# Kernel tuning notes

Measured on AMD Instinct MI355X. Metric: run time of the kernel, lower is better.

## Reference

```python
import jax, jax.numpy as jnp
import numpy as np

NUM_EMBEDDINGS = 1024
EMBEDDING_DIM = 64
COMMITMENT_WEIGHT = 0.25
BATCH = 262144


def setup_inputs() -> dict:
    key = jax.random.key(0)
    k1, k2 = jax.random.split(key)
    z = jax.random.normal(k1, (BATCH, EMBEDDING_DIM), dtype=jnp.float32)
    # torch init: uniform_(-1/K, 1/K)
    bound = 1.0 / NUM_EMBEDDINGS
    codebook = jax.random.uniform(k2, (NUM_EMBEDDINGS, EMBEDDING_DIM), dtype=jnp.float32,
                                  minval=-bound, maxval=bound)
    return {"z": z, "codebook": codebook}


def reference(z, codebook):
    # distances[b, k] = ||z_b||^2 - 2 z_b . c_k + ||c_k||^2   -> [B, K]
    z2 = jnp.sum(z * z, axis=1, keepdims=True)                 # [B, 1]
    c2 = jnp.sum(codebook * codebook, axis=1)                  # [K]
    cross = jnp.matmul(z, codebook.T)                          # [B, K]
    distances = z2 - 2.0 * cross + c2
    indices = jnp.argmin(distances, axis=1)                    # [B]
    # original uses one-hot @ codebook; direct gather is the same math
    z_q = codebook[indices]                                    # [B, D]
    commitment_loss = jnp.mean((jax.lax.stop_gradient(z_q) - z) ** 2)
    codebook_loss = jnp.mean((z_q - jax.lax.stop_gradient(z)) ** 2)
    vq_loss = codebook_loss + COMMITMENT_WEIGHT * commitment_loss
    # straight-through estimator
    z_q_st = z + jax.lax.stop_gradient(z_q - z)
    return z_q_st, vq_loss, indices
```

## Files before the change

kernel.cpp:

```cpp
#include <hip/hip_runtime.h>

#define BATCH   262144
#define NCODE   1024
#define DIM     64
#define BLOCK   256
#define NBLK    (BATCH / BLOCK)
#define MARGIN  4e-5f
#define QCAP    65536


typedef __attribute__((ext_vector_type(8))) short bf16x8;
typedef __attribute__((ext_vector_type(4))) float f32x4;

#define MFMA(a, b, c) __builtin_amdgcn_mfma_f32_16x16x32_bf16(a, b, c, 0, 0, 0)

__device__ __forceinline__ void split1(float f, unsigned short& h, unsigned short& l) {
    unsigned u = __float_as_uint(f);
    unsigned r = (u + 0x7fffu + ((u >> 16) & 1u)) >> 16;
    h = (unsigned short)r;
    float hf = __uint_as_float(r << 16);
    float lo = f - hf;
    unsigned u2 = __float_as_uint(lo);
    l = (unsigned short)((u2 + 0x7fffu + ((u2 >> 16) & 1u)) >> 16);
}

__global__ __launch_bounds__(256) void prep_kernel(
        const float* __restrict__ cb, float* __restrict__ c2,
        float* __restrict__ cbT, unsigned short* __restrict__ pack,
        unsigned int* __restrict__ qcount)
{
    const int gid = blockIdx.x * 256 + threadIdx.x;
    if (gid == 0) *qcount = 0u;
    cbT[(size_t)(gid & 63) * NCODE + (gid >> 6)] = cb[gid];
    if (gid < NCODE) {
        const float* row = cb + (size_t)gid * DIM;
        float r[8];
#pragma unroll
        for (int j = 0; j < 8; ++j) r[j] = __fmul_rn(row[j], row[j]);
#pragma unroll
        for (int i = 8; i < DIM; i += 8) {
#pragma unroll
            for (int j = 0; j < 8; ++j) r[j] = __fadd_rn(r[j], __fmul_rn(row[i + j], row[i + j]));
        }
        c2[gid] = __fadd_rn(__fadd_rn(__fadd_rn(r[0], r[1]), __fadd_rn(r[2], r[3])),
                            __fadd_rn(__fadd_rn(r[4], r[5]), __fadd_rn(r[6], r[7])));
    }
    if (gid < 4096) {
        const int t = gid >> 6, lane = gid & 63;
        const int c = t * 16 + (lane & 15);
        const int g = lane >> 4;
#pragma unroll
        for (int s = 0; s < 2; ++s) {
            const float* src = cb + (size_t)c * DIM + s * 32 + g * 8;
            bf16x8 hv, lv;
#pragma unroll
            for (int j = 0; j < 8; ++j) {
                unsigned short hh, ll; split1(src[j], hh, ll);
                hv[j] = (short)hh; lv[j] = (short)ll;
            }
            *(bf16x8*)(pack + ((size_t)(t * 4 + 2 * s + 0) * 64 + lane) * 8) = hv;
            *(bf16x8*)(pack + ((size_t)(t * 4 + 2 * s + 1) * 64 + lane) * 8) = lv;
        }
    }
}

__global__ __launch_bounds__(256) void screen_kernel(
        const float* __restrict__ z, const unsigned short* __restrict__ pack,
        const float* __restrict__ c2, float* __restrict__ out_idx,
        unsigned char* __restrict__ flags, int* __restrict__ queue,
        unsigned int* __restrict__ qcount)
{
    const int tid  = threadIdx.x;
    const int lane = tid & 63, wid = tid >> 6;
    const int col  = lane & 15, g = lane >> 4;
    const int rowbase = blockIdx.x * 256 + wid * 64;

    bf16x8 Ah[4][2], Al[4][2];
#pragma unroll
    for (int rt = 0; rt < 4; ++rt)
#pragma unroll
        for (int s = 0; s < 2; ++s) {
            const float* zp = z + (size_t)(rowbase + rt * 16 + col) * DIM + s * 32 + g * 8;
            float tmp[8];
            *(float4*)(tmp)     = ((const float4*)zp)[0];
            *(float4*)(tmp + 4) = ((const float4*)zp)[1];
            bf16x8 hv, lv;
#pragma unroll
            for (int j = 0; j < 8; ++j) {
                unsigned short hh, ll; split1(tmp[j], hh, ll);
                hv[j] = (short)hh; lv[j] = (short)ll;
            }
            Ah[rt][s] = hv; Al[rt][s] = lv;
        }

    float b1[16], b2[16], bk[16];
#pragma unroll
    for (int i = 0; i < 16; ++i) { b1[i] = __builtin_inff(); b2[i] = __builtin_inff(); bk[i] = 0.f; }
    float codef = (float)col;

#define UPD(i, sv) { const float s_ = (sv); \
                     bk[i] = (s_ < b1[i]) ? codef : bk[i]; \
                     b2[i] = __builtin_amdgcn_fmed3f(s_, b1[i], b2[i]); \
                     b1[i] = fminf(b1[i], s_); }

#pragma unroll 1
    for (int t8 = 0; t8 < 8; ++t8) {
        float c2r[8];
#pragma unroll
        for (int u = 0; u < 8; ++u) c2r[u] = c2[(t8 * 8 + u) * 16 + col];
#pragma unroll
        for (int u = 0; u < 8; ++u) {
            const unsigned short* bp = pack + (size_t)(t8 * 8 + u) * 2048;
            bf16x8 Bh0 = *(const bf16x8*)(bp +    0 + lane * 8);
            bf16x8 Bl0 = *(const bf16x8*)(bp +  512 + lane * 8);
            bf16x8 Bh1 = *(const bf16x8*)(bp + 1024 + lane * 8);
            bf16x8 Bl1 = *(const bf16x8*)(bp + 1536 + lane * 8);
            const float c2v = c2r[u];
#pragma unroll
            for (int rt = 0; rt < 4; ++rt) {
                f32x4 acc = {0.f, 0.f, 0.f, 0.f};
                acc = MFMA(Ah[rt][0], Bh0, acc); acc = MFMA(Ah[rt][1], Bh1, acc);
                acc = MFMA(Ah[rt][0], Bl0, acc); acc = MFMA(Al[rt][0], Bh0, acc);
                acc = MFMA(Ah[rt][1], Bl1, acc); acc = MFMA(Al[rt][1], Bh1, acc);
#pragma unroll
                for (int reg = 0; reg < 4; ++reg) {
                    UPD(rt * 4 + reg, __fmaf_rn(-2.0f, acc[reg], c2v));
                }
            }
            codef += 16.f;
        }
    }
#undef UPD

#pragma unroll
    for (int i = 0; i < 16; ++i) {
        float v1 = b1[i], v2 = b2[i], vk = bk[i];
#pragma unroll
        for (int m = 1; m < 16; m <<= 1) {
            const float o1 = __shfl_xor(v1, m);
            const float o2 = __shfl_xor(v2, m);
            const float ok = __shfl_xor(vk, m);
            v2 = fminf(fminf(v2, o2), fmaxf(v1, o1));
            if (o1 < v1) vk = ok;
            v1 = fminf(v1, o1);
        }
        if (col == 0) {
            const int rt = i >> 2, reg = i & 3;
            const int row = rowbase + rt * 16 + g * 4 + reg;
            out_idx[row] = vk;
            const bool f = (v2 - v1 <= MARGIN);
            flags[row] = f ? 1 : 0;
            if (f) {
                unsigned int p = atomicAdd(qcount, 1u);
                if (p < QCAP) queue[p] = row;
            }
        }
    }
}

__device__ void fix_row(int row, const float* __restrict__ z, const float* __restrict__ cbT,
                        const float* __restrict__ c2, float* __restrict__ out_idx,
                        float* zs, float* rv, int* ri)
{
    const int tid = threadIdx.x;
    __syncthreads();
    if (tid < 16) ((float4*)zs)[tid] = ((const float4*)(z + (size_t)row * DIM))[tid];
    __syncthreads();
    float ra[8];
#pragma unroll
    for (int j = 0; j < 8; ++j) ra[j] = __fmul_rn(zs[j], zs[j]);
#pragma unroll
    for (int d = 8; d < DIM; d += 8) {
#pragma unroll
        for (int j = 0; j < 8; ++j) ra[j] = __fadd_rn(ra[j], __fmul_rn(zs[d + j], zs[d + j]));
    }
    const float z2 = __fadd_rn(__fadd_rn(__fadd_rn(ra[0], ra[1]), __fadd_rn(ra[2], ra[3])),
                               __fadd_rn(__fadd_rn(ra[4], ra[5]), __fadd_rn(ra[6], ra[7])));
    float a[4] = {0.f, 0.f, 0.f, 0.f};
#pragma unroll 8
    for (int d = 0; d < DIM; ++d) {
        const float zd = zs[d];
        const float4 cv = ((const float4*)(cbT + (size_t)d * NCODE))[tid];
        a[0] = __fmaf_rn(zd, cv.x, a[0]);
        a[1] = __fmaf_rn(zd, cv.y, a[1]);
        a[2] = __fmaf_rn(zd, cv.z, a[2]);
        a[3] = __fmaf_rn(zd, cv.w, a[3]);
    }
    const int k0 = tid * 4;
    float best = __builtin_inff();
    int bestk = NCODE;
#pragma unroll
    for (int j = 0; j < 4; ++j) {
        const float dist = __fadd_rn(__fmaf_rn(-2.0f, a[j], z2), c2[k0 + j]);
        if (dist < best) { best = dist; bestk = k0 + j; }
    }
    rv[tid] = best; ri[tid] = bestk;
    __syncthreads();
#pragma unroll
    for (int s = 128; s > 0; s >>= 1) {
        if (tid < s) {
            const float ov = rv[tid + s]; const int oi = ri[tid + s];
            if (ov < rv[tid] || (ov == rv[tid] && oi < ri[tid])) { rv[tid] = ov; ri[tid] = oi; }
        }
        __syncthreads();
    }
    if (tid == 0) out_idx[row] = (float)ri[0];
}

__global__ __launch_bounds__(256) void fix_kernel(
        const float* __restrict__ z, const float* __restrict__ cbT,
        const float* __restrict__ c2, const int* __restrict__ queue,
        const unsigned int* __restrict__ qcount, const unsigned char* __restrict__ flags,
        float* __restrict__ out_idx)
{
    __shared__ float zs[DIM];
    __shared__ float rv[256];
    __shared__ int   ri[256];
    const unsigned int nq = *qcount;
    if (nq <= QCAP) {
        for (unsigned int qi = blockIdx.x; qi < nq; qi += gridDim.x)
            fix_row(queue[qi], z, cbT, c2, out_idx, zs, rv, ri);
    } else {
        for (int row = blockIdx.x; row < BATCH; row += (int)gridDim.x)
            if (flags[row]) fix_row(row, z, cbT, c2, out_idx, zs, rv, ri);
    }
}

__global__ __launch_bounds__(BLOCK) void emit_kernel(
        const float* __restrict__ z, const float* __restrict__ cb,
        const float* __restrict__ out_idx, float* __restrict__ out_zq,
        double* __restrict__ partial)
{
    const int b = blockIdx.x * BLOCK + threadIdx.x;
    const int bestk = (int)out_idx[b];
    const float* cq = cb + (size_t)bestk * DIM;
    const float4* zv = (const float4*)(z + (size_t)b * DIM);
    const float4* qv = (const float4*)cq;
    float4* ov = (float4*)(out_zq + (size_t)b * DIM);
    double lsum = 0.0;
#pragma unroll
    for (int i = 0; i < DIM / 4; ++i) {
        float4 qq = qv[i], zl = zv[i];
        float qa[4] = {qq.x, qq.y, qq.z, qq.w};
        float za[4] = {zl.x, zl.y, zl.z, zl.w};
        float o[4];
#pragma unroll
        for (int j = 0; j < 4; ++j) {
            const float t = __fsub_rn(qa[j], za[j]);
            o[j] = __fadd_rn(za[j], t);
            lsum += (double)t * (double)t;
        }
        float4 vv; vv.x = o[0]; vv.y = o[1]; vv.z = o[2]; vv.w = o[3];
        ov[i] = vv;
    }

    __shared__ double sred[BLOCK];
    sred[threadIdx.x] = lsum;
    __syncthreads();
#pragma unroll
    for (int s = BLOCK / 2; s > 0; s >>= 1) {
        if (threadIdx.x < s) sred[threadIdx.x] += sred[threadIdx.x + s];
        __syncthreads();
    }
    if (threadIdx.x == 0) partial[blockIdx.x] = sred[0];
}

__global__ void loss_kernel(const double* __restrict__ partial, float* __restrict__ out_loss) {
    __shared__ double sred[256];
    double s = 0.0;
    for (int i = threadIdx.x; i < NBLK; i += 256) s += partial[i];
    sred[threadIdx.x] = s;
    __syncthreads();
#pragma unroll
    for (int st = 128; st > 0; st >>= 1) {
        if (threadIdx.x < st) sred[threadIdx.x] += sred[threadIdx.x + st];
        __syncthreads();
    }
    if (threadIdx.x == 0) {
        const double mean = sred[0] / (double)((size_t)BATCH * DIM);
        const float L = (float)mean;
        out_loss[0] = __fadd_rn(L, __fmul_rn(0.25f, L));
    }
}

extern "C" void kernel_launch(void* const* d_in, const int* in_sizes, int n_in,
                              void* d_out, int out_size, void* d_ws, size_t ws_size,
                              hipStream_t stream) {
    (void)in_sizes; (void)n_in; (void)out_size; (void)ws_size;
    const float* z  = (const float*)d_in[0];
    const float* cb = (const float*)d_in[1];
    float* out      = (float*)d_out;
    float* out_zq   = out;
    float* out_loss = out + (size_t)BATCH * DIM;
    float* out_idx  = out + (size_t)BATCH * DIM + 1;
    double* partial = (double*)d_ws;
    float* c2       = (float*)((char*)d_ws + 8192);
    unsigned int* qcount = (unsigned int*)((char*)d_ws + 12288);
    unsigned char* flags = (unsigned char*)d_ws + 12544;
    unsigned short* pack = (unsigned short*)((char*)d_ws + 274688);
    int* queue      = (int*)((char*)d_ws + 536832);
    float* cbT      = (float*)((char*)d_ws + 798976);

    prep_kernel<<<256, 256, 0, stream>>>(cb, c2, cbT, pack, qcount);
    screen_kernel<<<BATCH / 256, 256, 0, stream>>>(z, pack, c2, out_idx, flags, queue, qcount);
    fix_kernel<<<2048, 256, 0, stream>>>(z, cbT, c2, queue, qcount, flags, out_idx);
    emit_kernel<<<NBLK, BLOCK, 0, stream>>>(z, cb, out_idx, out_zq, partial);
    loss_kernel<<<1, 256, 0, stream>>>(partial, out_loss);
}
```

Baseline: 340.7 us.

## Stage codebook through double-buffered LDS and fold norm into MFMA accumulator

The screen kernel now streams the packed bf16 hi/lo codebook into a double-buffered LDS tile using global_load_lds, overlapping the next chunk's load with the current chunk's MFMAs, instead of each wave reading it from global memory. The score becomes z·c - 0.5||c||^2, with the -0.5||c||^2 term preloaded into the accumulator, which removes the per-element FMA. Tracking changes from min to max, and each block now covers 128 rows (32 per wave) with half the accumulator state. The flags array is dropped, so the overflow fallback in the fix kernel now rescans every row, and the margin is rescaled to match the halved score.

```diff
diff --git a/kernel.cpp b/kernel.cpp
--- a/kernel.cpp
+++ b/kernel.cpp
@@ -5,7 +5,7 @@
 #define DIM     64
 #define BLOCK   256
 #define NBLK    (BATCH / BLOCK)
-#define MARGIN  4e-5f
+#define MARGIN2 2e-5f
 #define QCAP    65536
 
 
@@ -25,7 +25,7 @@
 }
 
 __global__ __launch_bounds__(256) void prep_kernel(
-        const float* __restrict__ cb, float* __restrict__ c2,
+        const float* __restrict__ cb, float* __restrict__ c2, float* __restrict__ c2n,
         float* __restrict__ cbT, unsigned short* __restrict__ pack,
         unsigned int* __restrict__ qcount)
 {
@@ -42,8 +42,10 @@
 #pragma unroll
             for (int j = 0; j < 8; ++j) r[j] = __fadd_rn(r[j], __fmul_rn(row[i + j], row[i + j]));
         }
-        c2[gid] = __fadd_rn(__fadd_rn(__fadd_rn(r[0], r[1]), __fadd_rn(r[2], r[3])),
-                            __fadd_rn(__fadd_rn(r[4], r[5]), __fadd_rn(r[6], r[7])));
+        const float v = __fadd_rn(__fadd_rn(__fadd_rn(r[0], r[1]), __fadd_rn(r[2], r[3])),
+                                  __fadd_rn(__fadd_rn(r[4], r[5]), __fadd_rn(r[6], r[7])));
+        c2[gid] = v;
+        c2n[gid] = -0.5f * v;
     }
     if (gid < 4096) {
         const int t = gid >> 6, lane = gid & 63;
@@ -66,18 +68,18 @@
 
 __global__ __launch_bounds__(256) void screen_kernel(
         const float* __restrict__ z, const unsigned short* __restrict__ pack,
-        const float* __restrict__ c2, float* __restrict__ out_idx,
-        unsigned char* __restrict__ flags, int* __restrict__ queue,
-        unsigned int* __restrict__ qcount)
-{
+        const float* __restrict__ c2n, float* __restrict__ out_idx,
+        int* __restrict__ queue, unsigned int* __restrict__ qcount)
+{
+    __shared__ __align__(16) unsigned short lds[2][8192];
     const int tid  = threadIdx.x;
     const int lane = tid & 63, wid = tid >> 6;
     const int col  = lane & 15, g = lane >> 4;
-    const int rowbase = blockIdx.x * 256 + wid * 64;
-
-    bf16x8 Ah[4][2], Al[4][2];
-#pragma unroll
-    for (int rt = 0; rt < 4; ++rt)
+    const int rowbase = blockIdx.x * 128 + wid * 32;
+
+    bf16x8 Ah[2][2], Al[2][2];
+#pragma unroll
+    for (int rt = 0; rt < 2; ++rt)
 #pragma unroll
         for (int s = 0; s < 2; ++s) {
             const float* zp = z + (size_t)(rowbase + rt * 16 + col) * DIM + s * 32 + g * 8;
@@ -93,64 +95,81 @@
             Ah[rt][s] = hv; Al[rt][s] = lv;
         }
 
-    float b1[16], b2[16], bk[16];
-#pragma unroll
-    for (int i = 0; i < 16; ++i) { b1[i] = __builtin_inff(); b2[i] = __builtin_inff(); bk[i] = 0.f; }
+    float b1[8], b2[8], bk[8];
+#pragma unroll
+    for (int i = 0; i < 8; ++i) {
+        b1[i] = -__builtin_inff(); b2[i] = -__builtin_inff(); bk[i] = 0.f;
+    }
     float codef = (float)col;
 
 #define UPD(i, sv) { const float s_ = (sv); \
-                     bk[i] = (s_ < b1[i]) ? codef : bk[i]; \
+                     bk[i] = (s_ > b1[i]) ? codef : bk[i]; \
                      b2[i] = __builtin_amdgcn_fmed3f(s_, b1[i], b2[i]); \
-                     b1[i] = fminf(b1[i], s_); }
-
+                     b1[i] = fmaxf(b1[i], s_); }
+
+#define STAGE(c, buf) { \
+_Pragma("unroll") \
+        for (int i_ = 0; i_ < 4; ++i_) { \
+            const int seg_ = wid * 4 + i_; \
+            const unsigned short* g_ = pack + (size_t)(c) * 8192 + seg_ * 512 + lane * 8; \
+            unsigned short* l_ = &lds[buf][seg_ * 512]; \
+            __builtin_amdgcn_global_load_lds( \
+                (const __attribute__((address_space(1))) unsigned int*)g_, \
+                (__attribute__((address_space(3))) unsigned int*)l_, 16, 0, 0); \
+        } }
+
+    int cur = 0;
+    STAGE(0, 0);
+    __syncthreads();
 #pragma unroll 1
-    for (int t8 = 0; t8 < 8; ++t8) {
-        float c2r[8];
-#pragma unroll
-        for (int u = 0; u < 8; ++u) c2r[u] = c2[(t8 * 8 + u) * 16 + col];
-#pragma unroll
-        for (int u = 0; u < 8; ++u) {
-            const unsigned short* bp = pack + (size_t)(t8 * 8 + u) * 2048;
-            bf16x8 Bh0 = *(const bf16x8*)(bp +    0 + lane * 8);
-            bf16x8 Bl0 = *(const bf16x8*)(bp +  512 + lane * 8);
-            bf16x8 Bh1 = *(const bf16x8*)(bp + 1024 + lane * 8);
-            bf16x8 Bl1 = *(const bf16x8*)(bp + 1536 + lane * 8);
-            const float c2v = c2r[u];
-#pragma unroll
-            for (int rt = 0; rt < 4; ++rt) {
-                f32x4 acc = {0.f, 0.f, 0.f, 0.f};
+    for (int c = 0; c < 16; ++c) {
+        if (c < 15) STAGE(c + 1, cur ^ 1);
+        float c2r[4];
+#pragma unroll
+        for (int u = 0; u < 4; ++u) c2r[u] = c2n[(c * 4 + u) * 16 + col];
+        const unsigned short* buf = &lds[cur][0];
+#pragma unroll
+        for (int u = 0; u < 4; ++u) {
+            const unsigned short* lb = buf + u * 2048;
+            bf16x8 Bh0 = *(const bf16x8*)(lb +    0 + lane * 8);
+            bf16x8 Bl0 = *(const bf16x8*)(lb +  512 + lane * 8);
+            bf16x8 Bh1 = *(const bf16x8*)(lb + 1024 + lane * 8);
+            bf16x8 Bl1 = *(const bf16x8*)(lb + 1536 + lane * 8);
+            const float cv = c2r[u];
+#pragma unroll
+            for (int rt = 0; rt < 2; ++rt) {
+                f32x4 acc = {cv, cv, cv, cv};
                 acc = MFMA(Ah[rt][0], Bh0, acc); acc = MFMA(Ah[rt][1], Bh1, acc);
                 acc = MFMA(Ah[rt][0], Bl0, acc); acc = MFMA(Al[rt][0], Bh0, acc);
                 acc = MFMA(Ah[rt][1], Bl1, acc); acc = MFMA(Al[rt][1], Bh1, acc);
 #pragma unroll
-                for (int reg = 0; reg < 4; ++reg) {
-                    UPD(rt * 4 + reg, __fmaf_rn(-2.0f, acc[reg], c2v));
-                }
+                for (int reg = 0; reg < 4; ++reg) UPD(rt * 4 + reg, acc[reg]);
             }
             codef += 16.f;
         }
+        __syncthreads();
+        cur ^= 1;
     }
 #undef UPD
-
-#pragma unroll
-    for (int i = 0; i < 16; ++i) {
+#undef STAGE
+
+#pragma unroll
+    for (int i = 0; i < 8; ++i) {
         float v1 = b1[i], v2 = b2[i], vk = bk[i];
 #pragma unroll
         for (int m = 1; m < 16; m <<= 1) {
             const float o1 = __shfl_xor(v1, m);
             const float o2 = __shfl_xor(v2, m);
             const float ok = __shfl_xor(vk, m);
-            v2 = fminf(fminf(v2, o2), fmaxf(v1, o1));
-            if (o1 < v1) vk = ok;
-            v1 = fminf(v1, o1);
+            v2 = fmaxf(fmaxf(v2, o2), fminf(v1, o1));
+            if (o1 > v1) vk = ok;
+            v1 = fmaxf(v1, o1);
         }
         if (col == 0) {
             const int rt = i >> 2, reg = i & 3;
             const int row = rowbase + rt * 16 + g * 4 + reg;
             out_idx[row] = vk;
-            const bool f = (v2 - v1 <= MARGIN);
-            flags[row] = f ? 1 : 0;
-            if (f) {
+            if (v1 - v2 <= MARGIN2) {
                 unsigned int p = atomicAdd(qcount, 1u);
                 if (p < QCAP) queue[p] = row;
             }
@@ -210,8 +229,7 @@
 __global__ __launch_bounds__(256) void fix_kernel(
         const float* __restrict__ z, const float* __restrict__ cbT,
         const float* __restrict__ c2, const int* __restrict__ queue,
-        const unsigned int* __restrict__ qcount, const unsigned char* __restrict__ flags,
-        float* __restrict__ out_idx)
+        const unsigned int* __restrict__ qcount, float* __restrict__ out_idx)
 {
     __shared__ float zs[DIM];
     __shared__ float rv[256];
@@ -222,7 +240,7 @@
             fix_row(queue[qi], z, cbT, c2, out_idx, zs, rv, ri);
     } else {
         for (int row = blockIdx.x; row < BATCH; row += (int)gridDim.x)
-            if (flags[row]) fix_row(row, z, cbT, c2, out_idx, zs, rv, ri);
+            fix_row(row, z, cbT, c2, out_idx, zs, rv, ri);
     }
 }
 
@@ -296,14 +314,14 @@
     double* partial = (double*)d_ws;
     float* c2       = (float*)((char*)d_ws + 8192);
     unsigned int* qcount = (unsigned int*)((char*)d_ws + 12288);
-    unsigned char* flags = (unsigned char*)d_ws + 12544;
-    unsigned short* pack = (unsigned short*)((char*)d_ws + 274688);
-    int* queue      = (int*)((char*)d_ws + 536832);
-    float* cbT      = (float*)((char*)d_ws + 798976);
-
-    prep_kernel<<<256, 256, 0, stream>>>(cb, c2, cbT, pack, qcount);
-    screen_kernel<<<BATCH / 256, 256, 0, stream>>>(z, pack, c2, out_idx, flags, queue, qcount);
-    fix_kernel<<<2048, 256, 0, stream>>>(z, cbT, c2, queue, qcount, flags, out_idx);
+    float* c2n      = (float*)((char*)d_ws + 12544);
+    unsigned short* pack = (unsigned short*)((char*)d_ws + 16640);
+    int* queue      = (int*)((char*)d_ws + 278784);
+    float* cbT      = (float*)((char*)d_ws + 540928);
+
+    prep_kernel<<<256, 256, 0, stream>>>(cb, c2, c2n, cbT, pack, qcount);
+    screen_kernel<<<BATCH / 128, 256, 0, stream>>>(z, pack, c2n, out_idx, queue, qcount);
+    fix_kernel<<<2048, 256, 0, stream>>>(z, cbT, c2, queue, qcount, out_idx);
     emit_kernel<<<NBLK, BLOCK, 0, stream>>>(z, cb, out_idx, out_zq, partial);
     loss_kernel<<<1, 256, 0, stream>>>(partial, out_loss);
 }
```

Result: faster. 307.1 us (-9.8%).
